# Performance work log

Measured on AMD Instinct MI355X. Metric: run time of the kernel, lower is better.

Reference implementation:

```python
import jax, jax.numpy as jnp
import numpy as np

EMBED_DIM = 1024
NUM_HEADS = 16
HEAD_DIM = EMBED_DIM // NUM_HEADS
B, L = 4, 2048


def _xavier(key, out_dim, in_dim):
    limit = jnp.sqrt(6.0 / (in_dim + out_dim))
    return jax.random.uniform(key, (out_dim, in_dim), jnp.float32, -limit, limit)


def setup_inputs() -> dict:
    key = jax.random.key(0)
    kx, kq, kk, kv, ko = jax.random.split(key, 5)
    return {
        "x": jax.random.normal(kx, (B, L, EMBED_DIM), jnp.float32),
        "Wq": _xavier(kq, EMBED_DIM, EMBED_DIM), "bq": jnp.zeros((EMBED_DIM,), jnp.float32),
        "Wk": _xavier(kk, EMBED_DIM, EMBED_DIM), "bk": jnp.zeros((EMBED_DIM,), jnp.float32),
        "Wv": _xavier(kv, EMBED_DIM, EMBED_DIM), "bv": jnp.zeros((EMBED_DIM,), jnp.float32),
        "Wo": _xavier(ko, EMBED_DIM, EMBED_DIM), "bo": jnp.zeros((EMBED_DIM,), jnp.float32),
    }


def reference(x, Wq, bq, Wk, bk, Wv, bv, Wo, bo):
    bs, l, e = x.shape
    h, hd = NUM_HEADS, HEAD_DIM
    # torch Linear: y = x @ W.T + b
    q = (x @ Wq.T + bq).reshape(bs, l, h, hd).transpose(0, 2, 1, 3)  # [b,h,l,hd]
    k = (x @ Wk.T + bk).reshape(bs, l, h, hd).transpose(0, 2, 1, 3)
    v = (x @ Wv.T + bv).reshape(bs, l, h, hd).transpose(0, 2, 1, 3)
    scale = 1.0 / jnp.sqrt(jnp.asarray(hd, x.dtype))
    scores = jnp.einsum("bhqd,bhkd->bhqk", q, k) * scale  # [b,h,l,l]
    attn = jax.nn.softmax(scores, axis=-1)
    out = jnp.einsum("bhqk,bhkd->bhqd", attn, v)  # [b,h,l,hd]
    out = out.transpose(0, 2, 1, 3).reshape(bs, l, e)
    return out @ Wo.T + bo
```

## Files before the change

### kernel.cpp

```cpp
#include <hip/hip_runtime.h>
#include <stdint.h>

#define NB 4
#define NL 2048
#define NE 1024
#define NH 16
#define ND 64
#define NM (NB*NL)

typedef float f32x4 __attribute__((ext_vector_type(4)));
typedef short s16x8 __attribute__((ext_vector_type(8)));

__device__ __forceinline__ unsigned short f2b(float f) {
  uint32_t u = __float_as_uint(f);
  u += 0x7fffu + ((u >> 16) & 1u);
  return (unsigned short)(u >> 16);
}

__device__ __forceinline__ void gload16(const void* g, void* l) {
  __builtin_amdgcn_global_load_lds((const __attribute__((address_space(1))) void*)g,
                                   (__attribute__((address_space(3))) void*)l, 16, 0, 0);
}

__global__ void cvt_kernel(const float* __restrict__ in, unsigned short* __restrict__ out, int n8) {
  int stride = gridDim.x * blockDim.x;
  for (int i = blockIdx.x * blockDim.x + threadIdx.x; i < n8; i += stride) {
    const float4* p = (const float4*)in + (size_t)i * 2;
    float4 a = p[0], b = p[1];
    s16x8 r;
    r[0] = (short)f2b(a.x); r[1] = (short)f2b(a.y); r[2] = (short)f2b(a.z); r[3] = (short)f2b(a.w);
    r[4] = (short)f2b(b.x); r[5] = (short)f2b(b.y); r[6] = (short)f2b(b.z); r[7] = (short)f2b(b.w);
    *((s16x8*)out + i) = r;
  }
}

__global__ void cvt4_kernel(const float* __restrict__ w0, const float* __restrict__ w1,
                            const float* __restrict__ w2, const float* __restrict__ w3,
                            unsigned short* __restrict__ o0, unsigned short* __restrict__ o1,
                            unsigned short* __restrict__ o2, unsigned short* __restrict__ o3,
                            int n8) {
  const int y = blockIdx.y;
  const float* in = (y == 0) ? w0 : (y == 1) ? w1 : (y == 2) ? w2 : w3;
  unsigned short* out = (y == 0) ? o0 : (y == 1) ? o1 : (y == 2) ? o2 : o3;
  int stride = gridDim.x * blockDim.x;
  for (int i = blockIdx.x * blockDim.x + threadIdx.x; i < n8; i += stride) {
    const float4* p = (const float4*)in + (size_t)i * 2;
    float4 a = p[0], b = p[1];
    s16x8 r;
    r[0] = (short)f2b(a.x); r[1] = (short)f2b(a.y); r[2] = (short)f2b(a.z); r[3] = (short)f2b(a.w);
    r[4] = (short)f2b(b.x); r[5] = (short)f2b(b.y); r[6] = (short)f2b(b.z); r[7] = (short)f2b(b.w);
    *((s16x8*)out + i) = r;
  }
}

template<int MODE>
__launch_bounds__(256, 2)
__global__ void gemm_bt(const unsigned short* __restrict__ A,
                        const unsigned short* __restrict__ W0,
                        const unsigned short* __restrict__ W1,
                        const unsigned short* __restrict__ W2,
                        const float* __restrict__ b0,
                        const float* __restrict__ b1,
                        const float* __restrict__ b2,
                        unsigned short* __restrict__ O0,
                        unsigned short* __restrict__ O1,
                        unsigned short* __restrict__ O2,
                        float* __restrict__ fout)
{
  __shared__ alignas(16) char smem[32768];
  char* sA = smem;
  char* sB = smem + 16384;

  const int tid = threadIdx.x;
  const int lane = tid & 63;
  const int wid = tid >> 6;
  const int bx = blockIdx.x, by = blockIdx.y;
  const int m0 = by * 128;

  int which = 0;
  const unsigned short* Wsel;
  const float* bias;
  int n0;
  if (MODE == 0) {
    which = bx >> 3;
    Wsel = (which == 0) ? W0 : ((which == 1) ? W1 : W2);
    bias = (which == 0) ? b0 : ((which == 1) ? b1 : b2);
    n0 = (bx & 7) * 128;
  } else {
    Wsel = W0; bias = b0; n0 = bx * 128;
  }

  const int wr = (wid >> 1) * 64;
  const int wc = (wid & 1) * 64;
  int aaddr[4], baddr[4];
#pragma unroll
  for (int m = 0; m < 4; ++m) {
    int ra = wr + m * 16 + (lane & 15);
    aaddr[m] = ra * 128 + (((lane >> 4) * 16) ^ ((ra & 7) << 4));
    int rb = wc + m * 16 + (lane & 15);
    baddr[m] = rb * 128 + (((lane >> 4) * 16) ^ ((rb & 7) << 4));
  }

  f32x4 acc[4][4] = {};
  const int c0 = wid * 64 + lane;

  for (int kt = 0; kt < 16; ++kt) {
    const int k0 = kt * 64;
#pragma unroll
    for (int it = 0; it < 4; ++it) {
      int c = it * 256 + c0;
      int row = c >> 3;
      int sb = ((((c & 7) << 4)) ^ ((row & 7) << 4)) >> 1;
      gload16(A    + (size_t)(m0 + row) * NE + k0 + sb, sA + it * 4096 + wid * 1024);
      gload16(Wsel + (size_t)(n0 + row) * NE + k0 + sb, sB + it * 4096 + wid * 1024);
    }
    __syncthreads();
#pragma unroll
    for (int kk = 0; kk < 2; ++kk) {
      s16x8 af[4], bf[4];
#pragma unroll
      for (int m = 0; m < 4; ++m) af[m] = *(const s16x8*)(sA + (aaddr[m] ^ (kk << 6)));
#pragma unroll
      for (int n = 0; n < 4; ++n) bf[n] = *(const s16x8*)(sB + (baddr[n] ^ (kk << 6)));
#pragma unroll
      for (int m = 0; m < 4; ++m)
#pragma unroll
        for (int n = 0; n < 4; ++n)
          acc[m][n] = __builtin_amdgcn_mfma_f32_16x16x32_bf16(af[m], bf[n], acc[m][n], 0, 0, 0);
    }
    __syncthreads();
  }

#pragma unroll
  for (int m = 0; m < 4; ++m) {
    const int row0 = m0 + wr + m * 16 + ((lane >> 4) << 2);
#pragma unroll
    for (int n = 0; n < 4; ++n) {
      const int col = n0 + wc + n * 16 + (lane & 15);
      const float bv = bias[col];
      if (MODE == 1) {
#pragma unroll
        for (int r = 0; r < 4; ++r)
          fout[(size_t)(row0 + r) * NE + col] = acc[m][n][r] + bv;
      } else {
        const int b = row0 >> 11;
        const int l = row0 & 2047;
        const int h = col >> 6;
        const int d = col & 63;
        if (which < 2) {
          unsigned short* dst = (which == 0) ? O0 : O1;
#pragma unroll
          for (int r = 0; r < 4; ++r)
            dst[((size_t)(b * NH + h) * NL + (l + r)) * ND + d] = f2b(acc[m][n][r] + bv);
        } else {
          ushort4 pk;
          pk.x = f2b(acc[m][n][0] + bv);
          pk.y = f2b(acc[m][n][1] + bv);
          pk.z = f2b(acc[m][n][2] + bv);
          pk.w = f2b(acc[m][n][3] + bv);
          *(ushort4*)(O2 + ((size_t)(b * NH + h) * ND + d) * NL + l) = pk;
        }
      }
    }
  }
}

__launch_bounds__(256, 2)
__global__ void attn_kernel(const unsigned short* __restrict__ Q,
                            const unsigned short* __restrict__ K,
                            const unsigned short* __restrict__ Vt,
                            unsigned short* __restrict__ AO)
{
  __shared__ alignas(16) char smem[65536];
  char* sK = smem;
  char* sV = smem + 16384;
  char* sP = smem + 32768;

  const int tid = threadIdx.x;
  const int lane = tid & 63;
  const int wid = tid >> 6;
  const int qt = blockIdx.x;
  const int bh = blockIdx.y;
  const int b = bh >> 4;
  const int h = bh & 15;
  const size_t base = (size_t)bh * NL * ND;
  const int q0 = qt * 128 + wid * 32;

  s16x8 qf[2][2];
#pragma unroll
  for (int m = 0; m < 2; ++m)
#pragma unroll
    for (int kk = 0; kk < 2; ++kk)
      qf[m][kk] = *(const s16x8*)(Q + base + (size_t)(q0 + m * 16 + (lane & 15)) * ND
                                  + kk * 32 + (lane >> 4) * 8);

  f32x4 o[2][4] = {};
  float rm[2][4], rl[2][4];
#pragma unroll
  for (int m = 0; m < 2; ++m)
#pragma unroll
    for (int r = 0; r < 4; ++r) { rm[m][r] = -1e30f; rl[m][r] = 0.f; }

  int kaddr[8], vaddr[4], paddr[2];
#pragma unroll
  for (int n = 0; n < 8; ++n) {
    int rk = n * 16 + (lane & 15);
    kaddr[n] = rk * 128 + (((lane >> 4) * 16) ^ ((rk & 7) << 4));
  }
#pragma unroll
  for (int n = 0; n < 4; ++n) {
    int rd = n * 16 + (lane & 15);
    vaddr[n] = rd * 256 + (((lane >> 4) * 16) ^ ((rd & 7) << 4));
  }
#pragma unroll
  for (int m = 0; m < 2; ++m) {
    int rp = m * 16 + (lane & 15);
    paddr[m] = wid * 8192 + rp * 256 + (((lane >> 4) * 16) ^ ((rp & 7) << 4));
  }
  const int c0 = wid * 64 + lane;
  const float SC = 0.125f * 1.44269504088896f;

  for (int t = 0; t < 16; ++t) {
    const int kv0 = t * 128;
#pragma unroll
    for (int it = 0; it < 4; ++it) {
      int c = it * 256 + c0;
      {
        int row = c >> 3;
        int sb = ((((c & 7) << 4)) ^ ((row & 7) << 4)) >> 1;
        gload16(K + base + (size_t)(kv0 + row) * ND + sb, sK + it * 4096 + wid * 1024);
      }
      {
        int d = c >> 4;
        int sb = ((((c & 15) << 4)) ^ ((d & 7) << 4)) >> 1;
        gload16(Vt + base + (size_t)d * NL + kv0 + sb, sV + it * 4096 + wid * 1024);
      }
    }
    __syncthreads();

    f32x4 s[2][8] = {};
#pragma unroll
    for (int kk = 0; kk < 2; ++kk) {
      s16x8 kf[8];
#pragma unroll
      for (int n = 0; n < 8; ++n) kf[n] = *(const s16x8*)(sK + (kaddr[n] ^ (kk << 6)));
#pragma unroll
      for (int m = 0; m < 2; ++m)
#pragma unroll
        for (int n = 0; n < 8; ++n)
          s[m][n] = __builtin_amdgcn_mfma_f32_16x16x32_bf16(qf[m][kk], kf[n], s[m][n], 0, 0, 0);
    }

#pragma unroll
    for (int m = 0; m < 2; ++m)
#pragma unroll
      for (int r = 0; r < 4; ++r) {
        float mx = s[m][0][r];
#pragma unroll
        for (int n = 1; n < 8; ++n) mx = fmaxf(mx, s[m][n][r]);
        mx *= SC;
#pragma unroll
        for (int off = 1; off < 16; off <<= 1) mx = fmaxf(mx, __shfl_xor(mx, off));
        float mnew = fmaxf(rm[m][r], mx);
        float alpha = __builtin_amdgcn_exp2f(rm[m][r] - mnew);
        rm[m][r] = mnew;
        float ts = 0.f;
        const int rr = m * 16 + ((lane >> 4) << 2) + r;
        const int pw = wid * 8192 + rr * 256;
        const int swz = (rr & 7) << 4;
#pragma unroll
        for (int n = 0; n < 8; ++n) {
          float p = __builtin_amdgcn_exp2f(s[m][n][r] * SC - mnew);
          ts += p;
          *(unsigned short*)(sP + pw + ((n * 32 + ((lane & 15) << 1)) ^ swz)) = f2b(p);
        }
#pragma unroll
        for (int off = 1; off < 16; off <<= 1) ts += __shfl_xor(ts, off);
        rl[m][r] = rl[m][r] * alpha + ts;
#pragma unroll
        for (int n = 0; n < 4; ++n) o[m][n][r] *= alpha;
      }

#pragma unroll
    for (int ks = 0; ks < 4; ++ks) {
      s16x8 pf[2], vf[4];
#pragma unroll
      for (int m = 0; m < 2; ++m) pf[m] = *(const s16x8*)(sP + (paddr[m] ^ (ks << 6)));
#pragma unroll
      for (int n = 0; n < 4; ++n) vf[n] = *(const s16x8*)(sV + (vaddr[n] ^ (ks << 6)));
#pragma unroll
      for (int m = 0; m < 2; ++m)
#pragma unroll
        for (int n = 0; n < 4; ++n)
          o[m][n] = __builtin_amdgcn_mfma_f32_16x16x32_bf16(pf[m], vf[n], o[m][n], 0, 0, 0);
    }
    __syncthreads();
  }

#pragma unroll
  for (int m = 0; m < 2; ++m)
#pragma unroll
    for (int r = 0; r < 4; ++r) {
      const float inv = 1.0f / rl[m][r];
      const int qrow = q0 + m * 16 + ((lane >> 4) << 2) + r;
#pragma unroll
      for (int n = 0; n < 4; ++n) {
        const int col = h * 64 + n * 16 + (lane & 15);
        AO[(size_t)(b * NL + qrow) * NE + col] = f2b(o[m][n][r] * inv);
      }
    }
}

extern "C" void kernel_launch(void* const* d_in, const int* in_sizes, int n_in,
                              void* d_out, int out_size, void* d_ws, size_t ws_size,
                              hipStream_t stream) {
  const float* x  = (const float*)d_in[0];
  const float* Wq = (const float*)d_in[1];
  const float* bq = (const float*)d_in[2];
  const float* Wk = (const float*)d_in[3];
  const float* bk = (const float*)d_in[4];
  const float* Wv = (const float*)d_in[5];
  const float* bv = (const float*)d_in[6];
  const float* Wo = (const float*)d_in[7];
  const float* bo = (const float*)d_in[8];
  float* out = (float*)d_out;
  char* ws = (char*)d_ws;

  unsigned short* xb  = (unsigned short*)(ws);
  unsigned short* AOw = (unsigned short*)(ws);
  unsigned short* wqb = (unsigned short*)(ws + (16u << 20));
  unsigned short* wkb = (unsigned short*)(ws + (18u << 20));
  unsigned short* wvb = (unsigned short*)(ws + (20u << 20));
  unsigned short* wob = (unsigned short*)(ws + (22u << 20));
  unsigned short* Qw  = (unsigned short*)(ws + (24u << 20));
  unsigned short* Kw  = (unsigned short*)(ws + (40u << 20));
  unsigned short* Vtw = (unsigned short*)(ws + (56u << 20));
  (void)in_sizes; (void)n_in; (void)out_size; (void)ws_size;

  cvt_kernel<<<1024, 256, 0, stream>>>(x, xb, (NM * NE) / 8);
  cvt4_kernel<<<dim3(128, 4), 256, 0, stream>>>(Wq, Wk, Wv, Wo,
                                                wqb, wkb, wvb, wob, (NE * NE) / 8);

  gemm_bt<0><<<dim3(24, 64), 256, 0, stream>>>(xb, wqb, wkb, wvb, bq, bk, bv,
                                               Qw, Kw, Vtw, nullptr);
  attn_kernel<<<dim3(16, 64), 256, 0, stream>>>(Qw, Kw, Vtw, AOw);
  gemm_bt<1><<<dim3(8, 64), 256, 0, stream>>>(AOw, wob, nullptr, nullptr, bo,
                                              nullptr, nullptr,
                                              nullptr, nullptr, nullptr, out);
}
```

Baseline: 360.9 us.

## Restructure attention: transposed S, double-buffered K/V, lazy rescale, folded Q scale

The attention kernel now computes S transposed (K as the A operand) so each lane holds a full query column. This turns the row max and sum reductions into two cross-lane shuffles instead of four. K/V tiles shrink to 64 keys and are double-buffered, prefetching the next tile while the current one is computed. The online softmax only rescales when the max grows by more than 8 (in log2 units), and the softmax scale times log2(e) is folded into Q in the projection GEMM epilogue. Launch bounds rise to 3 waves/blocks per SIMD and LDS drops to 48KB for higher occupancy, with P and output stored packed. The tradeoffs are register pressure from the tighter launch bound and some precision risk, since Q is scaled before bf16 rounding and rescaling is deferred.

```diff
diff --git a/kernel.cpp b/kernel.cpp
--- a/kernel.cpp
+++ b/kernel.cpp
@@ -15,6 +15,10 @@
   uint32_t u = __float_as_uint(f);
   u += 0x7fffu + ((u >> 16) & 1u);
   return (unsigned short)(u >> 16);
+}
+
+__device__ __forceinline__ uint32_t pk2(float a, float b) {
+  return (uint32_t)f2b(a) | ((uint32_t)f2b(b) << 16);
 }
 
 __device__ __forceinline__ void gload16(const void* g, void* l) {
@@ -54,7 +58,7 @@
 }
 
 template<int MODE>
-__launch_bounds__(256, 2)
+__launch_bounds__(256, 3)
 __global__ void gemm_bt(const unsigned short* __restrict__ A,
                         const unsigned short* __restrict__ W0,
                         const unsigned short* __restrict__ W1,
@@ -131,6 +135,7 @@
     __syncthreads();
   }
 
+  const float qsc = (MODE == 0 && ((bx >> 3) == 0)) ? 0.18033688011112042f : 1.0f;
 #pragma unroll
   for (int m = 0; m < 4; ++m) {
     const int row0 = m0 + wr + m * 16 + ((lane >> 4) << 2);
@@ -151,7 +156,7 @@
           unsigned short* dst = (which == 0) ? O0 : O1;
 #pragma unroll
           for (int r = 0; r < 4; ++r)
-            dst[((size_t)(b * NH + h) * NL + (l + r)) * ND + d] = f2b(acc[m][n][r] + bv);
+            dst[((size_t)(b * NH + h) * NL + (l + r)) * ND + d] = f2b((acc[m][n][r] + bv) * qsc);
         } else {
           ushort4 pk;
           pk.x = f2b(acc[m][n][0] + bv);
@@ -165,20 +170,19 @@
   }
 }
 
-__launch_bounds__(256, 2)
+__launch_bounds__(256, 3)
 __global__ void attn_kernel(const unsigned short* __restrict__ Q,
                             const unsigned short* __restrict__ K,
                             const unsigned short* __restrict__ Vt,
                             unsigned short* __restrict__ AO)
 {
-  __shared__ alignas(16) char smem[65536];
-  char* sK = smem;
-  char* sV = smem + 16384;
-  char* sP = smem + 32768;
+  __shared__ alignas(16) char smem[49152];
 
   const int tid = threadIdx.x;
   const int lane = tid & 63;
   const int wid = tid >> 6;
+  const int hi = lane >> 4;
+  const int qi = lane & 15;
   const int qt = blockIdx.x;
   const int bh = blockIdx.y;
   const int b = bh >> 4;
@@ -191,124 +195,135 @@
   for (int m = 0; m < 2; ++m)
 #pragma unroll
     for (int kk = 0; kk < 2; ++kk)
-      qf[m][kk] = *(const s16x8*)(Q + base + (size_t)(q0 + m * 16 + (lane & 15)) * ND
-                                  + kk * 32 + (lane >> 4) * 8);
+      qf[m][kk] = *(const s16x8*)(Q + base + (size_t)(q0 + m * 16 + qi) * ND
+                                  + kk * 32 + hi * 8);
 
   f32x4 o[2][4] = {};
-  float rm[2][4], rl[2][4];
-#pragma unroll
-  for (int m = 0; m < 2; ++m)
-#pragma unroll
-    for (int r = 0; r < 4; ++r) { rm[m][r] = -1e30f; rl[m][r] = 0.f; }
-
-  int kaddr[8], vaddr[4], paddr[2];
-#pragma unroll
-  for (int n = 0; n < 8; ++n) {
-    int rk = n * 16 + (lane & 15);
-    kaddr[n] = rk * 128 + (((lane >> 4) * 16) ^ ((rk & 7) << 4));
-  }
+  float rm[2] = {-1e30f, -1e30f};
+  float rl[2] = {0.f, 0.f};
+
+  int kaddr[4], vaddr[4];
 #pragma unroll
   for (int n = 0; n < 4; ++n) {
-    int rd = n * 16 + (lane & 15);
-    vaddr[n] = rd * 256 + (((lane >> 4) * 16) ^ ((rd & 7) << 4));
-  }
+    int rk = n * 16 + qi;
+    kaddr[n] = rk * 128 + ((hi * 16) ^ ((rk & 7) << 4));
+    vaddr[n] = kaddr[n];
+  }
+  char* sP = smem + 32768 + wid * 4096;
+  int pwoff[4], proff[2];
+#pragma unroll
+  for (int n = 0; n < 4; ++n)
+    pwoff[n] = qi * 128 + ((n * 32 + hi * 8) ^ ((qi & 7) << 4));
+#pragma unroll
+  for (int ks = 0; ks < 2; ++ks)
+    proff[ks] = qi * 128 + ((ks * 64 + hi * 16) ^ ((qi & 7) << 4));
+
+#define STAGE(T, BUF)                                                          \
+  do {                                                                         \
+    const int kv0_ = (T) * 64;                                                 \
+    char* sKb_ = smem + (BUF) * 8192;                                          \
+    char* sVb_ = smem + 16384 + (BUF) * 8192;                                  \
+    _Pragma("unroll")                                                          \
+    for (int it = 0; it < 2; ++it) {                                           \
+      int c = it * 256 + wid * 64 + lane;                                      \
+      int row = c >> 3;                                                        \
+      int sb = (((c & 7) << 4) ^ ((row & 7) << 4)) >> 1;                       \
+      gload16(K  + base + (size_t)(kv0_ + row) * ND + sb,                      \
+              sKb_ + it * 4096 + wid * 1024);                                  \
+      gload16(Vt + base + (size_t)row * NL + kv0_ + sb,                        \
+              sVb_ + it * 4096 + wid * 1024);                                  \
+    }                                                                          \
+  } while (0)
+
+  STAGE(0, 0);
+  __syncthreads();
+
+  for (int t = 0; t < 32; ++t) {
+    const int cur = t & 1;
+    if (t < 31) STAGE(t + 1, cur ^ 1);
+    const char* sKb = smem + cur * 8192;
+    const char* sVb = smem + 16384 + cur * 8192;
+
+    f32x4 s[2][4] = {};
+#pragma unroll
+    for (int kk = 0; kk < 2; ++kk) {
+      s16x8 kf[4];
+#pragma unroll
+      for (int n = 0; n < 4; ++n) kf[n] = *(const s16x8*)(sKb + (kaddr[n] ^ (kk << 6)));
+#pragma unroll
+      for (int m = 0; m < 2; ++m)
+#pragma unroll
+        for (int n = 0; n < 4; ++n)
+          s[m][n] = __builtin_amdgcn_mfma_f32_16x16x32_bf16(kf[n], qf[m][kk], s[m][n], 0, 0, 0);
+    }
+
+#pragma unroll
+    for (int m = 0; m < 2; ++m) {
+      float pm = s[m][0][0];
+#pragma unroll
+      for (int n = 0; n < 4; ++n)
+#pragma unroll
+        for (int r = 0; r < 4; ++r) pm = fmaxf(pm, s[m][n][r]);
+      pm = fmaxf(pm, __shfl_xor(pm, 16));
+      pm = fmaxf(pm, __shfl_xor(pm, 32));
+      float mn = rm[m];
+      if (!__all(pm - mn <= 8.0f)) {
+        mn = fmaxf(mn, pm);
+        float al = __builtin_amdgcn_exp2f(rm[m] - mn);
+        rl[m] *= al;
+#pragma unroll
+        for (int dt = 0; dt < 4; ++dt) o[m][dt] = o[m][dt] * al;
+        rm[m] = mn;
+      }
+      float ts = 0.f;
+#pragma unroll
+      for (int n = 0; n < 4; ++n) {
+        float p0 = __builtin_amdgcn_exp2f(s[m][n][0] - mn);
+        float p1 = __builtin_amdgcn_exp2f(s[m][n][1] - mn);
+        float p2 = __builtin_amdgcn_exp2f(s[m][n][2] - mn);
+        float p3 = __builtin_amdgcn_exp2f(s[m][n][3] - mn);
+        ts += (p0 + p1) + (p2 + p3);
+        uint2 w;
+        w.x = pk2(p0, p1);
+        w.y = pk2(p2, p3);
+        *(uint2*)(sP + m * 2048 + pwoff[n]) = w;
+      }
+      ts += __shfl_xor(ts, 16);
+      ts += __shfl_xor(ts, 32);
+      rl[m] += ts;
+    }
+
+#pragma unroll
+    for (int ks = 0; ks < 2; ++ks) {
+      s16x8 vf[4];
+#pragma unroll
+      for (int dt = 0; dt < 4; ++dt) vf[dt] = *(const s16x8*)(sVb + (vaddr[dt] ^ (ks << 6)));
+#pragma unroll
+      for (int m = 0; m < 2; ++m) {
+        s16x8 pf = *(const s16x8*)(sP + m * 2048 + proff[ks]);
+#pragma unroll
+        for (int dt = 0; dt < 4; ++dt)
+          o[m][dt] = __builtin_amdgcn_mfma_f32_16x16x32_bf16(vf[dt], pf, o[m][dt], 0, 0, 0);
+      }
+    }
+    __syncthreads();
+  }
+#undef STAGE
+
 #pragma unroll
   for (int m = 0; m < 2; ++m) {
-    int rp = m * 16 + (lane & 15);
-    paddr[m] = wid * 8192 + rp * 256 + (((lane >> 4) * 16) ^ ((rp & 7) << 4));
-  }
-  const int c0 = wid * 64 + lane;
-  const float SC = 0.125f * 1.44269504088896f;
-
-  for (int t = 0; t < 16; ++t) {
-    const int kv0 = t * 128;
-#pragma unroll
-    for (int it = 0; it < 4; ++it) {
-      int c = it * 256 + c0;
-      {
-        int row = c >> 3;
-        int sb = ((((c & 7) << 4)) ^ ((row & 7) << 4)) >> 1;
-        gload16(K + base + (size_t)(kv0 + row) * ND + sb, sK + it * 4096 + wid * 1024);
-      }
-      {
-        int d = c >> 4;
-        int sb = ((((c & 15) << 4)) ^ ((d & 7) << 4)) >> 1;
-        gload16(Vt + base + (size_t)d * NL + kv0 + sb, sV + it * 4096 + wid * 1024);
-      }
-    }
-    __syncthreads();
-
-    f32x4 s[2][8] = {};
-#pragma unroll
-    for (int kk = 0; kk < 2; ++kk) {
-      s16x8 kf[8];
-#pragma unroll
-      for (int n = 0; n < 8; ++n) kf[n] = *(const s16x8*)(sK + (kaddr[n] ^ (kk << 6)));
-#pragma unroll
-      for (int m = 0; m < 2; ++m)
-#pragma unroll
-        for (int n = 0; n < 8; ++n)
-          s[m][n] = __builtin_amdgcn_mfma_f32_16x16x32_bf16(qf[m][kk], kf[n], s[m][n], 0, 0, 0);
-    }
-
-#pragma unroll
-    for (int m = 0; m < 2; ++m)
-#pragma unroll
-      for (int r = 0; r < 4; ++r) {
-        float mx = s[m][0][r];
-#pragma unroll
-        for (int n = 1; n < 8; ++n) mx = fmaxf(mx, s[m][n][r]);
-        mx *= SC;
-#pragma unroll
-        for (int off = 1; off < 16; off <<= 1) mx = fmaxf(mx, __shfl_xor(mx, off));
-        float mnew = fmaxf(rm[m][r], mx);
-        float alpha = __builtin_amdgcn_exp2f(rm[m][r] - mnew);
-        rm[m][r] = mnew;
-        float ts = 0.f;
-        const int rr = m * 16 + ((lane >> 4) << 2) + r;
-        const int pw = wid * 8192 + rr * 256;
-        const int swz = (rr & 7) << 4;
-#pragma unroll
-        for (int n = 0; n < 8; ++n) {
-          float p = __builtin_amdgcn_exp2f(s[m][n][r] * SC - mnew);
-          ts += p;
-          *(unsigned short*)(sP + pw + ((n * 32 + ((lane & 15) << 1)) ^ swz)) = f2b(p);
-        }
-#pragma unroll
-        for (int off = 1; off < 16; off <<= 1) ts += __shfl_xor(ts, off);
-        rl[m][r] = rl[m][r] * alpha + ts;
-#pragma unroll
-        for (int n = 0; n < 4; ++n) o[m][n][r] *= alpha;
-      }
-
-#pragma unroll
-    for (int ks = 0; ks < 4; ++ks) {
-      s16x8 pf[2], vf[4];
-#pragma unroll
-      for (int m = 0; m < 2; ++m) pf[m] = *(const s16x8*)(sP + (paddr[m] ^ (ks << 6)));
-#pragma unroll
-      for (int n = 0; n < 4; ++n) vf[n] = *(const s16x8*)(sV + (vaddr[n] ^ (ks << 6)));
-#pragma unroll
-      for (int m = 0; m < 2; ++m)
-#pragma unroll
-        for (int n = 0; n < 4; ++n)
-          o[m][n] = __builtin_amdgcn_mfma_f32_16x16x32_bf16(pf[m], vf[n], o[m][n], 0, 0, 0);
-    }
-    __syncthreads();
-  }
-
-#pragma unroll
-  for (int m = 0; m < 2; ++m)
-#pragma unroll
-    for (int r = 0; r < 4; ++r) {
-      const float inv = 1.0f / rl[m][r];
-      const int qrow = q0 + m * 16 + ((lane >> 4) << 2) + r;
-#pragma unroll
-      for (int n = 0; n < 4; ++n) {
-        const int col = h * 64 + n * 16 + (lane & 15);
-        AO[(size_t)(b * NL + qrow) * NE + col] = f2b(o[m][n][r] * inv);
-      }
-    }
+    const float inv = 1.0f / rl[m];
+    const int qg = q0 + m * 16 + qi;
+#pragma unroll
+    for (int dt = 0; dt < 4; ++dt) {
+      ushort4 pk;
+      pk.x = f2b(o[m][dt][0] * inv);
+      pk.y = f2b(o[m][dt][1] * inv);
+      pk.z = f2b(o[m][dt][2] * inv);
+      pk.w = f2b(o[m][dt][3] * inv);
+      *(ushort4*)(AO + (size_t)(b * NL + qg) * NE + h * 64 + dt * 16 + hi * 4) = pk;
+    }
+  }
 }
 
 extern "C" void kernel_launch(void* const* d_in, const int* in_sizes, int n_in,
```

After: 313.6 us. 1.15x faster.
